# Performance work log

Hardware: AMD Instinct MI355X
Metric: run time of the kernel (lower is better)

Reference implementation:

```python
import jax, jax.numpy as jnp
import numpy as np
from math import sqrt

HEADS = 16
DIM_HEAD = 64
EPS = 1e-4
MP_T = 0.3


def l2norm(t, eps=EPS):
    n = jnp.linalg.norm(t, axis=-1, keepdims=True)
    return t / jnp.maximum(n, eps)


def mp_linear(x, w):
    # weight-normalized linear: l2norm rows / sqrt(fan_in)
    fan_in = w.shape[1]
    wn = l2norm(w) / sqrt(fan_in)
    return x @ wn.T


def setup_inputs() -> dict:
    key = jax.random.key(0)
    k1, k2, k3, k4 = jax.random.split(key, 4)
    b, n, dim = 2, 2048, 1024
    x = jax.random.normal(k1, (b, n, dim), dtype=jnp.float32)
    w_qkv = jax.random.normal(k2, (3 * HEADS * DIM_HEAD, dim), dtype=jnp.float32)
    w_out = jax.random.normal(k3, (dim, HEADS * DIM_HEAD), dtype=jnp.float32)
    mem_kv = jax.random.normal(k4, (2, HEADS, 4, DIM_HEAD), dtype=jnp.float32)
    return {"x": x, "w_qkv": w_qkv, "w_out": w_out, "mem_kv": mem_kv}


def reference(x, w_qkv, w_out, mem_kv):
    b, n, dim = x.shape
    h, d = HEADS, DIM_HEAD
    scale = d ** -0.5

    qkv = mp_linear(x, w_qkv)                      # [b, n, 3*h*d]
    q, k, v = jnp.split(qkv, 3, axis=-1)
    split_heads = lambda t: t.reshape(b, n, h, d).transpose(0, 2, 1, 3)  # b h n d
    q, k, v = map(split_heads, (q, k, v))

    mk = jnp.broadcast_to(mem_kv[0], (b, h, mem_kv.shape[2], d))
    mv = jnp.broadcast_to(mem_kv[1], (b, h, mem_kv.shape[2], d))
    k = jnp.concatenate([mk, k], axis=2)
    v = jnp.concatenate([mv, v], axis=2)

    # pixel_norm: l2 normalize over head dim, rescale by sqrt(d)
    pn = lambda t: l2norm(t) * sqrt(d)
    q, k, v = pn(q), pn(k), pn(v)

    q = q * scale
    sim = jnp.einsum('bhid,bhjd->bhij', q, k)
    attn = jax.nn.softmax(sim, axis=-1)
    out = jnp.einsum('bhij,bhjd->bhid', attn, v)
    out = out.transpose(0, 2, 1, 3).reshape(b, n, h * d)
    out = mp_linear(out, w_out)

    # magnitude-preserving residual add
    t = MP_T
    return (out * (1.0 - t) + x * t) / sqrt((1.0 - t) ** 2 + t ** 2)
```

## Files before the change

kernel.cpp:

```cpp
#include <hip/hip_runtime.h>
#include <hip/hip_bf16.h>
#include <math.h>


#define EPSN 1e-4f
#define LDH 72
#define NKEY 2112
#define LOG2E 1.4426950408889634f

typedef __attribute__((ext_vector_type(8))) short short8;
typedef __attribute__((ext_vector_type(4))) short short4v;
typedef __attribute__((ext_vector_type(4))) float floatx4;

typedef __attribute__((address_space(1))) const void g_void;
typedef __attribute__((address_space(3))) void lds_void;

__device__ __forceinline__ void async16(void* lds, const void* g) {
    __builtin_amdgcn_global_load_lds((g_void*)g, (lds_void*)lds, 16, 0, 0);
}

__device__ __forceinline__ short f2bf(float f) {
    union { float f; unsigned u; } c{f};
    unsigned r = (c.u + 0x7FFF + ((c.u >> 16) & 1)) >> 16;
    return (short)r;
}
__device__ __forceinline__ short f2bf_fast(float f) {
    union { float f; unsigned u; } c{f};
    return (short)((c.u + 0x8000) >> 16);
}

__global__ __launch_bounds__(256) void prep_inputs(const float* __restrict__ x,
                                                   const float* __restrict__ w_qkv,
                                                   const float* __restrict__ w_out,
                                                   const float* __restrict__ memkv,
                                                   short* __restrict__ xb,
                                                   short* __restrict__ wnqkv,
                                                   short* __restrict__ wnout,
                                                   short* __restrict__ Kb,
                                                   short* __restrict__ Vt) {
    const int bid = blockIdx.x, tid = threadIdx.x;
    if (bid < 4096) {
        int i = bid * 1024 + tid * 4;
        float4 v = *(const float4*)(x + i);
        short4v s = {f2bf(v.x), f2bf(v.y), f2bf(v.z), f2bf(v.w)};
        *(short4v*)(xb + i) = s;
        return;
    }
    if (bid < 8192) {
        const float* w; short* wn; int r;
        if (bid < 7168) { w = w_qkv; wn = wnqkv; r = bid - 4096; }
        else            { w = w_out; wn = wnout; r = bid - 7168; }
        __shared__ float red[256];
        const float* row = w + (size_t)r * 1024;
        float ss = 0.f;
        for (int c = tid; c < 1024; c += 256) { float v = row[c]; ss += v * v; }
        red[tid] = ss;
        __syncthreads();
        for (int s = 128; s > 0; s >>= 1) {
            if (tid < s) red[tid] += red[tid + s];
            __syncthreads();
        }
        float f = 1.0f / (fmaxf(sqrtf(red[0]), EPSN) * 32.0f);
        for (int c = tid; c < 1024; c += 256) wn[(size_t)r * 1024 + c] = f2bf(row[c] * f);
        return;
    }
    const int bh = bid - 8192, h = bh & 15;
    const int r = tid >> 2, part = tid & 3;
    if (r < 4) {
        const float* pk = memkv + (size_t)(h * 4 + r) * 64 + part * 16;
        const float* pv = memkv + (size_t)((16 + h) * 4 + r) * 64 + part * 16;
        float k[16], v[16]; float ssk = 0.f, ssv = 0.f;
        #pragma unroll
        for (int i = 0; i < 16; i += 4) {
            float4 a = *(const float4*)(pk + i);
            float4 b = *(const float4*)(pv + i);
            k[i]=a.x; k[i+1]=a.y; k[i+2]=a.z; k[i+3]=a.w;
            v[i]=b.x; v[i+1]=b.y; v[i+2]=b.z; v[i+3]=b.w;
            ssk += a.x*a.x + a.y*a.y + a.z*a.z + a.w*a.w;
            ssv += b.x*b.x + b.y*b.y + b.z*b.z + b.w*b.w;
        }
        ssk += __shfl_xor(ssk, 1); ssk += __shfl_xor(ssk, 2);
        ssv += __shfl_xor(ssv, 1); ssv += __shfl_xor(ssv, 2);
        const float fk = 8.0f / fmaxf(sqrtf(ssk), EPSN);
        const float fv = 8.0f / fmaxf(sqrtf(ssv), EPSN);
        short* kd = Kb + ((size_t)bh * NKEY + r) * 64 + part * 16;
        #pragma unroll
        for (int i = 0; i < 16; i++) kd[i] = f2bf(k[i] * fk);
        #pragma unroll
        for (int i = 0; i < 16; i++)
            Vt[((size_t)bh * 64 + part * 16 + i) * NKEY + r] = f2bf(v[i] * fv);
    }
    for (int p = tid; p < 480; p += 256)
        *(short8*)(Kb + ((size_t)bh * NKEY + 2052) * 64 + p * 8) = (short8){0,0,0,0,0,0,0,0};
    for (int p = tid; p < 960; p += 256) {
        int row = p / 15, c = p % 15;
        *(short4v*)(Vt + ((size_t)bh * 64 + row) * NKEY + 2052 + c * 4) = (short4v){0,0,0,0};
    }
}

__global__ __launch_bounds__(256) void gemm_qkv(const short* __restrict__ A,
                                                const short* __restrict__ B,
                                                short* __restrict__ Qb,
                                                short* __restrict__ Kb,
                                                short* __restrict__ Vt) {
    constexpr int K = 1024;
    __shared__ __align__(16) short As[2][128 * 32];
    __shared__ __align__(16) short Bs[2][128 * 32];
    const int tid = threadIdx.x;
    const int wv = tid >> 6, lane = tid & 63;
    const int l16 = lane & 15, quad = lane >> 4;
    const int wr = wv >> 1, wc = wv & 1;
    const int bm0 = blockIdx.y * 128, bn0 = blockIdx.x * 128;
    const int grow = lane >> 2;
    const int gk = (lane & 3) * 8;

    floatx4 acc[4][4];
    #pragma unroll
    for (int i = 0; i < 4; i++)
        #pragma unroll
        for (int j = 0; j < 4; j++) acc[i][j] = (floatx4){0.f, 0.f, 0.f, 0.f};

    const short* Abase = A + (size_t)(bm0 + wv * 32 + grow) * K + gk;
    const short* Bbase = B + (size_t)(bn0 + wv * 32 + grow) * K + gk;

    #pragma unroll
    for (int j = 0; j < 2; j++) {
        async16(&As[0][(wv * 32 + j * 16) * 32], Abase + (size_t)(j * 16) * K);
        async16(&Bs[0][(wv * 32 + j * 16) * 32], Bbase + (size_t)(j * 16) * K);
    }
    const int NKI = K >> 5;
    for (int ki = 0; ki < NKI; ki++) {
        const int cur = ki & 1;
        if (ki + 1 < NKI) {
            const int nxt = cur ^ 1;
            const int off = (ki + 1) * 32;
            #pragma unroll
            for (int j = 0; j < 2; j++) {
                async16(&As[nxt][(wv * 32 + j * 16) * 32], Abase + (size_t)(j * 16) * K + off);
                async16(&Bs[nxt][(wv * 32 + j * 16) * 32], Bbase + (size_t)(j * 16) * K + off);
            }
            asm volatile("s_waitcnt vmcnt(4)" ::: "memory");
        } else {
            asm volatile("s_waitcnt vmcnt(0)" ::: "memory");
        }
        asm volatile("s_barrier" ::: "memory");
        short8 aA[4], bB[4];
        #pragma unroll
        for (int i = 0; i < 4; i++)
            aA[i] = *(const short8*)&As[cur][(wr * 64 + i * 16 + l16) * 32 + quad * 8];
        #pragma unroll
        for (int j = 0; j < 4; j++)
            bB[j] = *(const short8*)&Bs[cur][(wc * 64 + j * 16 + l16) * 32 + quad * 8];
        #pragma unroll
        for (int i = 0; i < 4; i++)
            #pragma unroll
            for (int j = 0; j < 4; j++)
                acc[i][j] = __builtin_amdgcn_mfma_f32_16x16x32_bf16(aA[i], bB[j], acc[i][j], 0, 0, 0);
        asm volatile("s_barrier" ::: "memory");
    }

    const int colbase = bn0 + wc * 64;
    const int which = colbase >> 10;
    const int h = (colbase >> 6) & 15;
    float sc[4][4];
    #pragma unroll
    for (int i = 0; i < 4; i++)
        #pragma unroll
        for (int r = 0; r < 4; r++) {
            float ss = 0.f;
            #pragma unroll
            for (int j = 0; j < 4; j++) ss += acc[i][j][r] * acc[i][j][r];
            ss += __shfl_xor(ss, 1); ss += __shfl_xor(ss, 2);
            ss += __shfl_xor(ss, 4); ss += __shfl_xor(ss, 8);
            const float num = (which == 0) ? LOG2E : 8.0f;
            sc[i][r] = num / fmaxf(sqrtf(ss), EPSN);
        }
    if (which == 2) {
        #pragma unroll
        for (int i = 0; i < 4; i++) {
            const int row0 = bm0 + wr * 64 + i * 16 + quad * 4;
            const int bh = (row0 >> 11) * 16 + h;
            const int tok0 = row0 & 2047;
            #pragma unroll
            for (int j = 0; j < 4; j++) {
                const int d = j * 16 + l16;
                short4v o = {f2bf(acc[i][j][0] * sc[i][0]), f2bf(acc[i][j][1] * sc[i][1]),
                             f2bf(acc[i][j][2] * sc[i][2]), f2bf(acc[i][j][3] * sc[i][3])};
                *(short4v*)(Vt + ((size_t)bh * 64 + d) * NKEY + 4 + tok0) = o;
            }
        }
    } else {
        #pragma unroll
        for (int i = 0; i < 4; i++)
            #pragma unroll
            for (int r = 0; r < 4; r++) {
                const int row = bm0 + wr * 64 + i * 16 + quad * 4 + r;
                const int bh = (row >> 11) * 16 + h;
                const int tok = row & 2047;
                const size_t base = (which == 0) ? ((size_t)bh * 2048 + tok) * 64
                                                 : ((size_t)bh * NKEY + 4 + tok) * 64;
                short* dst = (which == 0) ? Qb : Kb;
                #pragma unroll
                for (int j = 0; j < 4; j++)
                    dst[base + j * 16 + l16] = f2bf(acc[i][j][r] * sc[i][r]);
            }
    }
}

template<int MT, int NT>
__global__ __launch_bounds__(256) void gemm_mfma(const short* __restrict__ A,
                                                 const short* __restrict__ B,
                                                 float* __restrict__ C,
                                                 int M, int N, int K,
                                                 const float* __restrict__ resid) {
    constexpr int FI = MT / 32;
    constexpr int FJ = NT / 32;
    constexpr int nA = MT / 64;
    constexpr int nB = NT / 64;
    __shared__ __align__(16) short As[2][MT * 32];
    __shared__ __align__(16) short Bs[2][NT * 32];
    const int tid = threadIdx.x;
    const int wv = tid >> 6, lane = tid & 63;
    const int l16 = lane & 15, quad = lane >> 4;
    const int wr = wv >> 1, wc = wv & 1;
    const int bm0 = blockIdx.y * MT, bn0 = blockIdx.x * NT;
    const int grow = lane >> 2;
    const int gk = (lane & 3) * 8;

    floatx4 acc[FI][FJ];
    #pragma unroll
    for (int i = 0; i < FI; i++)
        #pragma unroll
        for (int j = 0; j < FJ; j++) acc[i][j] = (floatx4){0.f, 0.f, 0.f, 0.f};

    const short* Abase = A + (size_t)(bm0 + wv * (MT / 4) + grow) * K + gk;
    const short* Bbase = B + (size_t)(bn0 + wv * (NT / 4) + grow) * K + gk;

    #pragma unroll
    for (int j = 0; j < nA; j++)
        async16(&As[0][(wv * (MT / 4) + j * 16) * 32], Abase + (size_t)(j * 16) * K);
    #pragma unroll
    for (int j = 0; j < nB; j++)
        async16(&Bs[0][(wv * (NT / 4) + j * 16) * 32], Bbase + (size_t)(j * 16) * K);

    const int NKI = K >> 5;
    for (int ki = 0; ki < NKI; ki++) {
        const int cur = ki & 1;
        if (ki + 1 < NKI) {
            const int nxt = cur ^ 1;
            const int off = (ki + 1) * 32;
            #pragma unroll
            for (int j = 0; j < nA; j++)
                async16(&As[nxt][(wv * (MT / 4) + j * 16) * 32], Abase + (size_t)(j * 16) * K + off);
            #pragma unroll
            for (int j = 0; j < nB; j++)
                async16(&Bs[nxt][(wv * (NT / 4) + j * 16) * 32], Bbase + (size_t)(j * 16) * K + off);
            if constexpr (nA + nB == 4)      asm volatile("s_waitcnt vmcnt(4)" ::: "memory");
            else if constexpr (nA + nB == 3) asm volatile("s_waitcnt vmcnt(3)" ::: "memory");
            else                             asm volatile("s_waitcnt vmcnt(2)" ::: "memory");
        } else {
            asm volatile("s_waitcnt vmcnt(0)" ::: "memory");
        }
        asm volatile("s_barrier" ::: "memory");
        short8 aA[FI], bB[FJ];
        #pragma unroll
        for (int i = 0; i < FI; i++)
            aA[i] = *(const short8*)&As[cur][(wr * (MT / 2) + i * 16 + l16) * 32 + quad * 8];
        #pragma unroll
        for (int j = 0; j < FJ; j++)
            bB[j] = *(const short8*)&Bs[cur][(wc * (NT / 2) + j * 16 + l16) * 32 + quad * 8];
        #pragma unroll
        for (int i = 0; i < FI; i++)
            #pragma unroll
            for (int j = 0; j < FJ; j++)
                acc[i][j] = __builtin_amdgcn_mfma_f32_16x16x32_bf16(aA[i], bB[j], acc[i][j], 0, 0, 0);
        asm volatile("s_barrier" ::: "memory");
    }
    #pragma unroll
    for (int i = 0; i < FI; i++)
        #pragma unroll
        for (int j = 0; j < FJ; j++)
            #pragma unroll
            for (int r = 0; r < 4; r++) {
                const int row = bm0 + wr * (MT / 2) + i * 16 + quad * 4 + r;
                const int col = bn0 + wc * (NT / 2) + j * 16 + l16;
                const size_t idx = (size_t)row * N + col;
                float v = acc[i][j][r];
                if (resid) v = (v * 0.7f + resid[idx] * 0.3f) * 1.3130643285972254f;
                C[idx] = v;
            }
}

__global__ __launch_bounds__(512) void attn_mfma(const short* __restrict__ Qb,
                                                 const short* __restrict__ Kb,
                                                 const short* __restrict__ Vt,
                                                 short* __restrict__ out) {
    const int bh = blockIdx.x;
    const int q0 = blockIdx.y * 128;
    const int tid = threadIdx.x;
    const int wave = tid >> 6, lane = tid & 63;
    const int l16 = lane & 15, quad = lane >> 4;

    __shared__ __align__(16) short Ks2[2][2][64 * 32];
    __shared__ __align__(16) short Vs2[2][2][64 * 32];
    __shared__ __align__(16) short Ps[8][16 * LDH];

    const short* qp = Qb + ((size_t)bh * 2048 + q0 + wave * 16 + l16) * 64 + quad * 8;
    short8 aQ0 = *(const short8*)qp;
    short8 aQ1 = *(const short8*)(qp + 32);
    asm volatile("s_waitcnt vmcnt(0)" ::: "memory");

    const int grow = lane >> 2, gsub = (lane & 3) * 8;
    const int u0 = wave * 2;
    auto issue = [&](int tile, int buf) {
        #pragma unroll
        for (int s = 0; s < 2; s++) {
            const int u = u0 + s;
            const int hh = (u >> 2) & 1;
            const int L = u & 3;
            const int rr = L * 16 + grow;
            const int cc = hh * 32 + gsub;
            if (u < 8)
                async16(&Ks2[buf][hh][L * 512],
                        Kb + ((size_t)bh * NKEY + tile * 64 + rr) * 64 + cc);
            else
                async16(&Vs2[buf][hh][L * 512],
                        Vt + ((size_t)bh * 64 + rr) * NKEY + tile * 64 + cc);
        }
    };

    floatx4 O[4];
    #pragma unroll
    for (int t = 0; t < 4; t++) O[t] = (floatx4){0.f, 0.f, 0.f, 0.f};
    float lp[4] = {0.f, 0.f, 0.f, 0.f};

    issue(0, 0);
    for (int tile = 0; tile < 33; tile++) {
        const int cur = tile & 1;
        if (tile < 32) {
            issue(tile + 1, cur ^ 1);
            asm volatile("s_waitcnt vmcnt(2)" ::: "memory");
        } else {
            asm volatile("s_waitcnt vmcnt(0)" ::: "memory");
        }
        asm volatile("s_barrier" ::: "memory");

        floatx4 S[4];
        #pragma unroll
        for (int t = 0; t < 4; t++) {
            short8 b0 = *(const short8*)&Ks2[cur][0][(t * 16 + l16) * 32 + quad * 8];
            short8 b1 = *(const short8*)&Ks2[cur][1][(t * 16 + l16) * 32 + quad * 8];
            floatx4 s = (floatx4){-12.f, -12.f, -12.f, -12.f};
            s = __builtin_amdgcn_mfma_f32_16x16x32_bf16(aQ0, b0, s, 0, 0, 0);
            s = __builtin_amdgcn_mfma_f32_16x16x32_bf16(aQ1, b1, s, 0, 0, 0);
            S[t] = s;
        }
        if (tile == 32) {
            #pragma unroll
            for (int t = 0; t < 4; t++)
                if (t * 16 + l16 >= 4) { S[t][0] = S[t][1] = S[t][2] = S[t][3] = -1e30f; }
        }
        short* pp = Ps[wave];
        #pragma unroll
        for (int t = 0; t < 4; t++) {
            #pragma unroll
            for (int i = 0; i < 4; i++) {
                float p = __builtin_amdgcn_exp2f(S[t][i]);
                lp[i] += p;
                pp[(quad * 4 + i) * LDH + t * 16 + l16] = f2bf_fast(p);
            }
        }
        short8 aP0, aP1;
        {
            const short* pa = &pp[l16 * LDH + quad * 8];
            aP0 = *(const short8*)pa;
            aP1 = *(const short8*)(pa + 32);
        }
        #pragma unroll
        for (int t = 0; t < 4; t++) {
            short8 b0 = *(const short8*)&Vs2[cur][0][(t * 16 + l16) * 32 + quad * 8];
            short8 b1 = *(const short8*)&Vs2[cur][1][(t * 16 + l16) * 32 + quad * 8];
            O[t] = __builtin_amdgcn_mfma_f32_16x16x32_bf16(aP0, b0, O[t], 0, 0, 0);
            O[t] = __builtin_amdgcn_mfma_f32_16x16x32_bf16(aP1, b1, O[t], 0, 0, 0);
        }
        asm volatile("s_barrier" ::: "memory");
    }

    const int bb = bh >> 4, h = bh & 15;
    #pragma unroll
    for (int i = 0; i < 4; i++) {
        float s = lp[i];
        s += __shfl_xor(s, 1); s += __shfl_xor(s, 2);
        s += __shfl_xor(s, 4); s += __shfl_xor(s, 8);
        const float inv = 1.0f / s;
        const int qrow = q0 + wave * 16 + quad * 4 + i;
        const size_t base = ((size_t)(bb * 2048 + qrow)) * 1024 + h * 64 + l16;
        #pragma unroll
        for (int t = 0; t < 4; t++) out[base + t * 16] = f2bf(O[t][i] * inv);
    }
}

extern "C" void kernel_launch(void* const* d_in, const int* in_sizes, int n_in,
                              void* d_out, int out_size, void* d_ws, size_t ws_size,
                              hipStream_t stream) {
    const float* x      = (const float*)d_in[0];
    const float* w_qkv  = (const float*)d_in[1];
    const float* w_out  = (const float*)d_in[2];
    const float* mem_kv = (const float*)d_in[3];
    float* out = (float*)d_out;

    char* ws = (char*)d_ws;
    short* wnqkv_b = (short*)(ws);
    short* wnout_b = (short*)(ws + (6u << 20));
    short* xb      = (short*)(ws + (8u << 20));
    short* Qb      = (short*)(ws + (16u << 20));
    short* Kb      = (short*)(ws + (24u << 20));
    short* Vt      = (short*)(ws + (33u << 20));
    short* attnb   = (short*)(ws + (42u << 20));

    prep_inputs<<<8224, 256, 0, stream>>>(x, w_qkv, w_out, mem_kv,
                                          xb, wnqkv_b, wnout_b, Kb, Vt);

    gemm_qkv<<<dim3(3072 / 128, 4096 / 128), 256, 0, stream>>>(
        xb, wnqkv_b, Qb, Kb, Vt);

    attn_mfma<<<dim3(32, 16), 512, 0, stream>>>(Qb, Kb, Vt, attnb);

    gemm_mfma<128, 64><<<dim3(1024 / 64, 4096 / 128), 256, 0, stream>>>(
        attnb, wnout_b, out, 4096, 1024, 1024, x);
}
```

Baseline: 215.9 us.

## Restructure attention to 4 waves with 32 queries each and transposed MFMA operands

The attention kernel drops from 8 waves of 16 queries to 4 waves of 32 queries per block. It swaps the MFMA operand roles so that K and V are the A operand and Q and P are the B operand. Each K/V fragment read from LDS now feeds two query groups, which halves LDS fragment reads per unit of work. It also allows vectorized short4 writes of P and of the output, and the row-sum reduction becomes a cross-quad shuffle. The cost is more accumulator registers per wave and fewer waves per block to hide latency.

```diff
diff --git a/kernel.cpp b/kernel.cpp
--- a/kernel.cpp
+++ b/kernel.cpp
@@ -4,7 +4,6 @@
 
 
 #define EPSN 1e-4f
-#define LDH 72
 #define NKEY 2112
 #define LOG2E 1.4426950408889634f
 
@@ -291,7 +290,7 @@
             }
 }
 
-__global__ __launch_bounds__(512) void attn_mfma(const short* __restrict__ Qb,
+__global__ __launch_bounds__(256) void attn_mfma(const short* __restrict__ Qb,
                                                  const short* __restrict__ Kb,
                                                  const short* __restrict__ Vt,
                                                  short* __restrict__ out) {
@@ -303,101 +302,123 @@
 
     __shared__ __align__(16) short Ks2[2][2][64 * 32];
     __shared__ __align__(16) short Vs2[2][2][64 * 32];
-    __shared__ __align__(16) short Ps[8][16 * LDH];
-
-    const short* qp = Qb + ((size_t)bh * 2048 + q0 + wave * 16 + l16) * 64 + quad * 8;
-    short8 aQ0 = *(const short8*)qp;
-    short8 aQ1 = *(const short8*)(qp + 32);
+    __shared__ __align__(16) short Pw[4][32 * 72];
+
+    const short* qbase = Qb + ((size_t)bh * 2048 + q0 + wave * 32 + l16) * 64;
+    short8 bQ[2][2];
+    #pragma unroll
+    for (int qg = 0; qg < 2; qg++)
+        #pragma unroll
+        for (int dh = 0; dh < 2; dh++)
+            bQ[qg][dh] = *(const short8*)(qbase + qg * 1024 + dh * 32 + quad * 8);
     asm volatile("s_waitcnt vmcnt(0)" ::: "memory");
 
     const int grow = lane >> 2, gsub = (lane & 3) * 8;
-    const int u0 = wave * 2;
     auto issue = [&](int tile, int buf) {
         #pragma unroll
-        for (int s = 0; s < 2; s++) {
-            const int u = u0 + s;
-            const int hh = (u >> 2) & 1;
-            const int L = u & 3;
-            const int rr = L * 16 + grow;
-            const int cc = hh * 32 + gsub;
-            if (u < 8)
-                async16(&Ks2[buf][hh][L * 512],
-                        Kb + ((size_t)bh * NKEY + tile * 64 + rr) * 64 + cc);
-            else
-                async16(&Vs2[buf][hh][L * 512],
-                        Vt + ((size_t)bh * 64 + rr) * NKEY + tile * 64 + cc);
+        for (int s = 0; s < 4; s++) {
+            const int u = wave * 4 + s;
+            if (u < 8) {
+                const int dh = u >> 2, kc = u & 3;
+                async16(&Ks2[buf][dh][kc * 512],
+                        Kb + ((size_t)bh * NKEY + tile * 64 + kc * 16 + grow) * 64 + dh * 32 + gsub);
+            } else {
+                const int v = u - 8;
+                const int kh = v >> 2, dc = v & 3;
+                async16(&Vs2[buf][kh][dc * 512],
+                        Vt + ((size_t)bh * 64 + dc * 16 + grow) * NKEY + tile * 64 + kh * 32 + gsub);
+            }
         }
     };
 
-    floatx4 O[4];
-    #pragma unroll
-    for (int t = 0; t < 4; t++) O[t] = (floatx4){0.f, 0.f, 0.f, 0.f};
-    float lp[4] = {0.f, 0.f, 0.f, 0.f};
+    floatx4 O[4][2];
+    #pragma unroll
+    for (int dt = 0; dt < 4; dt++)
+        #pragma unroll
+        for (int qg = 0; qg < 2; qg++) O[dt][qg] = (floatx4){0.f, 0.f, 0.f, 0.f};
+    float lp[2] = {0.f, 0.f};
 
     issue(0, 0);
     for (int tile = 0; tile < 33; tile++) {
         const int cur = tile & 1;
         if (tile < 32) {
             issue(tile + 1, cur ^ 1);
-            asm volatile("s_waitcnt vmcnt(2)" ::: "memory");
+            asm volatile("s_waitcnt vmcnt(4)" ::: "memory");
         } else {
             asm volatile("s_waitcnt vmcnt(0)" ::: "memory");
         }
         asm volatile("s_barrier" ::: "memory");
 
-        floatx4 S[4];
-        #pragma unroll
-        for (int t = 0; t < 4; t++) {
-            short8 b0 = *(const short8*)&Ks2[cur][0][(t * 16 + l16) * 32 + quad * 8];
-            short8 b1 = *(const short8*)&Ks2[cur][1][(t * 16 + l16) * 32 + quad * 8];
-            floatx4 s = (floatx4){-12.f, -12.f, -12.f, -12.f};
-            s = __builtin_amdgcn_mfma_f32_16x16x32_bf16(aQ0, b0, s, 0, 0, 0);
-            s = __builtin_amdgcn_mfma_f32_16x16x32_bf16(aQ1, b1, s, 0, 0, 0);
-            S[t] = s;
+        floatx4 S[4][2];
+        #pragma unroll
+        for (int kt = 0; kt < 4; kt++) {
+            short8 aK0 = *(const short8*)&Ks2[cur][0][(kt * 16 + l16) * 32 + quad * 8];
+            short8 aK1 = *(const short8*)&Ks2[cur][1][(kt * 16 + l16) * 32 + quad * 8];
+            #pragma unroll
+            for (int qg = 0; qg < 2; qg++) {
+                floatx4 s = (floatx4){-12.f, -12.f, -12.f, -12.f};
+                s = __builtin_amdgcn_mfma_f32_16x16x32_bf16(aK0, bQ[qg][0], s, 0, 0, 0);
+                s = __builtin_amdgcn_mfma_f32_16x16x32_bf16(aK1, bQ[qg][1], s, 0, 0, 0);
+                S[kt][qg] = s;
+            }
         }
         if (tile == 32) {
             #pragma unroll
-            for (int t = 0; t < 4; t++)
-                if (t * 16 + l16 >= 4) { S[t][0] = S[t][1] = S[t][2] = S[t][3] = -1e30f; }
-        }
-        short* pp = Ps[wave];
-        #pragma unroll
-        for (int t = 0; t < 4; t++) {
-            #pragma unroll
-            for (int i = 0; i < 4; i++) {
-                float p = __builtin_amdgcn_exp2f(S[t][i]);
-                lp[i] += p;
-                pp[(quad * 4 + i) * LDH + t * 16 + l16] = f2bf_fast(p);
-            }
-        }
-        short8 aP0, aP1;
-        {
-            const short* pa = &pp[l16 * LDH + quad * 8];
-            aP0 = *(const short8*)pa;
-            aP1 = *(const short8*)(pa + 32);
-        }
-        #pragma unroll
-        for (int t = 0; t < 4; t++) {
-            short8 b0 = *(const short8*)&Vs2[cur][0][(t * 16 + l16) * 32 + quad * 8];
-            short8 b1 = *(const short8*)&Vs2[cur][1][(t * 16 + l16) * 32 + quad * 8];
-            O[t] = __builtin_amdgcn_mfma_f32_16x16x32_bf16(aP0, b0, O[t], 0, 0, 0);
-            O[t] = __builtin_amdgcn_mfma_f32_16x16x32_bf16(aP1, b1, O[t], 0, 0, 0);
+            for (int kt = 0; kt < 4; kt++)
+                #pragma unroll
+                for (int qg = 0; qg < 2; qg++)
+                    if (kt > 0 || quad > 0)
+                        S[kt][qg] = (floatx4){-1e30f, -1e30f, -1e30f, -1e30f};
+        }
+        #pragma unroll
+        for (int kt = 0; kt < 4; kt++)
+            #pragma unroll
+            for (int qg = 0; qg < 2; qg++) {
+                float p0 = __builtin_amdgcn_exp2f(S[kt][qg][0]);
+                float p1 = __builtin_amdgcn_exp2f(S[kt][qg][1]);
+                float p2 = __builtin_amdgcn_exp2f(S[kt][qg][2]);
+                float p3 = __builtin_amdgcn_exp2f(S[kt][qg][3]);
+                lp[qg] += (p0 + p1) + (p2 + p3);
+                short4v pk = {f2bf_fast(p0), f2bf_fast(p1), f2bf_fast(p2), f2bf_fast(p3)};
+                *(short4v*)&Pw[wave][(qg * 16 + l16) * 72 + kt * 16 + quad * 4] = pk;
+            }
+        short8 bP[2][2];
+        #pragma unroll
+        for (int qg = 0; qg < 2; qg++)
+            #pragma unroll
+            for (int kh = 0; kh < 2; kh++)
+                bP[qg][kh] = *(const short8*)&Pw[wave][(qg * 16 + l16) * 72 + kh * 32 + quad * 8];
+        #pragma unroll
+        for (int dt = 0; dt < 4; dt++) {
+            short8 aV0 = *(const short8*)&Vs2[cur][0][(dt * 16 + l16) * 32 + quad * 8];
+            short8 aV1 = *(const short8*)&Vs2[cur][1][(dt * 16 + l16) * 32 + quad * 8];
+            #pragma unroll
+            for (int qg = 0; qg < 2; qg++) {
+                O[dt][qg] = __builtin_amdgcn_mfma_f32_16x16x32_bf16(aV0, bP[qg][0], O[dt][qg], 0, 0, 0);
+                O[dt][qg] = __builtin_amdgcn_mfma_f32_16x16x32_bf16(aV1, bP[qg][1], O[dt][qg], 0, 0, 0);
+            }
         }
         asm volatile("s_barrier" ::: "memory");
     }
 
     const int bb = bh >> 4, h = bh & 15;
-    #pragma unroll
-    for (int i = 0; i < 4; i++) {
-        float s = lp[i];
-        s += __shfl_xor(s, 1); s += __shfl_xor(s, 2);
-        s += __shfl_xor(s, 4); s += __shfl_xor(s, 8);
-        const float inv = 1.0f / s;
-        const int qrow = q0 + wave * 16 + quad * 4 + i;
-        const size_t base = ((size_t)(bb * 2048 + qrow)) * 1024 + h * 64 + l16;
-        #pragma unroll
-        for (int t = 0; t < 4; t++) out[base + t * 16] = f2bf(O[t][i] * inv);
-    }
+    float inv[2];
+    #pragma unroll
+    for (int qg = 0; qg < 2; qg++) {
+        float l = lp[qg];
+        l += __shfl_xor(l, 16);
+        l += __shfl_xor(l, 32);
+        inv[qg] = 1.0f / l;
+    }
+    #pragma unroll
+    for (int dt = 0; dt < 4; dt++)
+        #pragma unroll
+        for (int qg = 0; qg < 2; qg++) {
+            const int token = q0 + wave * 32 + qg * 16 + l16;
+            short4v o = {f2bf(O[dt][qg][0] * inv[qg]), f2bf(O[dt][qg][1] * inv[qg]),
+                         f2bf(O[dt][qg][2] * inv[qg]), f2bf(O[dt][qg][3] * inv[qg])};
+            *(short4v*)(out + ((size_t)(bb * 2048 + token)) * 1024 + h * 64 + dt * 16 + quad * 4) = o;
+        }
 }
 
 extern "C" void kernel_launch(void* const* d_in, const int* in_sizes, int n_in,
@@ -424,7 +445,7 @@
     gemm_qkv<<<dim3(3072 / 128, 4096 / 128), 256, 0, stream>>>(
         xb, wnqkv_b, Qb, Kb, Vt);
 
-    attn_mfma<<<dim3(32, 16), 512, 0, stream>>>(Qb, Kb, Vt, attnb);
+    attn_mfma<<<dim3(32, 16), 256, 0, stream>>>(Qb, Kb, Vt, attnb);
 
     gemm_mfma<128, 64><<<dim3(1024 / 64, 4096 / 128), 256, 0, stream>>>(
         attnb, wnout_b, out, 4096, 1024, 1024, x);
```

New measurement: 212.5 us. Within noise of the previous version (-1.6%).
